# Kernel tuning notes

Measured on AMD Instinct MI355X. Metric: run time of the kernel, lower is better.

Reference implementation:

```python
import jax, jax.numpy as jnp
import numpy as np

B, V, D, H, ET = 32, 50, 6, 256, 4  # batch, num_vars, input_size, decoder_hidden, num_edge_types
E = V * (V - 1)                      # fully connected, no self-loops


def setup_inputs() -> dict:
    key = jax.random.key(0)
    ks = jax.random.split(key, 24)
    s = 0.05
    n = lambda k, shape: jax.random.normal(k, shape, jnp.float32)
    return {
        "inputs": n(ks[0], (B, V, D)),
        "hidden": n(ks[1], (B, V, H)),
        "edges": jax.random.uniform(ks[2], (B, E, ET), jnp.float32),
        # stacked per-edge-type message MLPs for the non-skipped types 1..ET-1
        "W1": n(ks[3], (ET - 1, H, 2 * H)) * s, "b1": jnp.full((ET - 1, H), 0.1, jnp.float32),
        "W2": n(ks[4], (ET - 1, H, H)) * s, "b2": jnp.full((ET - 1, H), 0.1, jnp.float32),
        # GRU-style update (hidden_* have no bias in the torch module)
        "Whr": n(ks[5], (H, H)) * s, "Whi": n(ks[6], (H, H)) * s, "Whh": n(ks[7], (H, H)) * s,
        "Wir": n(ks[8], (H, D)) * s, "bir": jnp.full((H,), 0.1, jnp.float32),
        "Wii": n(ks[9], (H, D)) * s, "bii": jnp.full((H,), 0.1, jnp.float32),
        "Win": n(ks[10], (H, D)) * s, "bin_w": jnp.full((H,), 0.1, jnp.float32),
        # output MLP
        "Wo1": n(ks[11], (H, H)) * s, "bo1": jnp.full((H,), 0.1, jnp.float32),
        "Wo2": n(ks[12], (H, H)) * s, "bo2": jnp.full((H,), 0.1, jnp.float32),
        "Wo3": n(ks[13], (D, H)) * s, "bo3": jnp.full((D,), 0.1, jnp.float32),
    }


def _edge_index(num_vars):
    mask = np.ones((num_vars, num_vars)) - np.eye(num_vars)
    send, recv = np.where(mask)
    onehot = np.zeros((send.shape[0], num_vars), dtype=np.float32)
    onehot[np.arange(send.shape[0]), recv] = 1.0  # edge2node scatter matrix [E, V]
    return send, recv, onehot


def reference(inputs, hidden, edges, W1, b1, W2, b2, Whr, Whi, Whh,
              Wir, bir, Wii, bii, Win, bin_w, Wo1, bo1, Wo2, bo2, Wo3, bo3):
    num_vars = hidden.shape[1]
    send, recv, onehot = _edge_index(num_vars)
    onehot = jnp.asarray(onehot)

    # gather: [B, E, 2H]
    pre_msg = jnp.concatenate([hidden[:, recv, :], hidden[:, send, :]], axis=-1)

    # per-edge-type message MLP (dropout is identity in eval mode), types 1..ET-1 (skip_first)
    m = jnp.tanh(jnp.einsum('bef,thf->bteh', pre_msg, W1) + b1[None, :, None, :])
    m = jnp.tanh(jnp.einsum('bteh,tgh->bteg', m, W2) + b2[None, :, None, :])
    ew = jnp.moveaxis(edges[:, :, 1:], -1, 1)          # [B, T, E]
    norm = edges.shape[-1] - 1
    all_msgs = jnp.einsum('bteh,bte->beh', m, ew) / norm  # [B, E, H]

    # scatter-aggregate edges -> receiver nodes
    agg = jnp.einsum('beh,ev->bvh', all_msgs, onehot) / (num_vars - 1)  # [B, V, H]

    # GRU-style gated update
    r = jax.nn.sigmoid(inputs @ Wir.T + bir + agg @ Whr.T)
    i = jax.nn.sigmoid(inputs @ Wii.T + bii + agg @ Whi.T)
    n_ = jnp.tanh(inputs @ Win.T + bin_w + r * (agg @ Whh.T))
    hidden_new = (1 - i) * n_ + i * hidden

    # output MLP with residual on inputs
    p = jax.nn.relu(hidden_new @ Wo1.T + bo1)
    p = jax.nn.relu(p @ Wo2.T + bo2)
    pred = inputs + (p @ Wo3.T + bo3)
    return pred, hidden_new
```

## Files before the change

### kernel.cpp

```cpp
#include <hip/hip_runtime.h>
#include <hip/hip_bf16.h>
#include <math.h>

#define B_ 32
#define V_ 50
#define D_ 6
#define H_ 256
#define E_ 2450
#define T_ 3
#define NN 1600
#define CHUNKS 39

#define OFF_inputs 0
#define OFF_hidden 9600
#define OFF_edges  419200
#define OFF_W1     732800
#define OFF_b1     1126016
#define OFF_W2     1126784
#define OFF_b2     1323392
#define OFF_Whr    1324160
#define OFF_Whi    1389696
#define OFF_Whh    1455232
#define OFF_Wir    1520768
#define OFF_bir    1522304
#define OFF_Wii    1522560
#define OFF_bii    1524096
#define OFF_Win    1524352
#define OFF_binw   1525888
#define OFF_Wo1    1526144
#define OFF_bo1    1591680
#define OFF_Wo2    1591936
#define OFF_bo2    1657472
#define OFF_Wo3    1657728
#define OFF_bo3    1659264
#define TOTAL_IN   1659270

#define PW_W2   0
#define PW_W1   196608
#define PW_WG   589824
#define PW_WO1  786432
#define PW_WO2  851968
#define PW_HID  917504
#define PW_TOT  1327104
#define AGG_N   409600

typedef __attribute__((ext_vector_type(8))) short short8;
typedef __attribute__((ext_vector_type(4))) float f32x4;

__device__ __forceinline__ float bfc(unsigned int u) {
    return __uint_as_float((u & 0xffffu) << 16);
}
__device__ __forceinline__ unsigned short f2bf(float f) {
    return __builtin_bit_cast(unsigned short, __float2bfloat16(f));
}
__device__ __forceinline__ float tanh_fast(float x) {
    float e = __builtin_amdgcn_exp2f(x * 2.8853900817779268f);
    return 1.0f - 2.0f * __builtin_amdgcn_rcpf(1.0f + e);
}
__device__ __forceinline__ float sigmoid_fast(float x) {
    float e = __builtin_amdgcn_exp2f(x * -1.4426950408889634f);
    return __builtin_amdgcn_rcpf(1.0f + e);
}

struct Ptrs { const void* p[22]; };

__device__ __forceinline__ int detect_bf(const Ptrs& pt) {
    const unsigned short* b1r = (const unsigned short*)pt.p[4];
    return (b1r[0] == 0x3DCDu && b1r[1] == 0x3DCDu) ? 1 : 0;
}
__device__ __forceinline__ float ldraw(const Ptrs& pt, int bf, int ti, int li) {
    return bf ? bfc(((const unsigned short*)pt.p[ti])[li])
              : ((const float*)pt.p[ti])[li];
}

__global__ __launch_bounds__(256) void kprepA(Ptrs pt, float* __restrict__ stag,
                                              unsigned short* __restrict__ W2s,
                                              unsigned short* __restrict__ W1s,
                                              unsigned short* __restrict__ Wgs,
                                              unsigned short* __restrict__ Wo1s,
                                              unsigned short* __restrict__ Wo2s,
                                              unsigned short* __restrict__ hidbf,
                                              float* __restrict__ aggf) {
    int i = blockIdx.x * 256 + threadIdx.x;
    if (i >= TOTAL_IN + PW_TOT + AGG_N) return;
    int bf = detect_bf(pt);
    if (i < TOTAL_IN) {
        int ti, base;
        if      (i < OFF_hidden) { ti = 0;  base = OFF_inputs; }
        else if (i < OFF_edges)  { ti = 1;  base = OFF_hidden; }
        else if (i < OFF_W1)     { ti = 2;  base = OFF_edges;  }
        else if (i < OFF_b1)     { ti = 3;  base = OFF_W1;     }
        else if (i < OFF_W2)     { ti = 4;  base = OFF_b1;     }
        else if (i < OFF_b2)     { ti = 5;  base = OFF_W2;     }
        else if (i < OFF_Whr)    { ti = 6;  base = OFF_b2;     }
        else if (i < OFF_Whi)    { ti = 7;  base = OFF_Whr;    }
        else if (i < OFF_Whh)    { ti = 8;  base = OFF_Whi;    }
        else if (i < OFF_Wir)    { ti = 9;  base = OFF_Whh;    }
        else if (i < OFF_bir)    { ti = 10; base = OFF_Wir;    }
        else if (i < OFF_Wii)    { ti = 11; base = OFF_bir;    }
        else if (i < OFF_bii)    { ti = 12; base = OFF_Wii;    }
        else if (i < OFF_Win)    { ti = 13; base = OFF_bii;    }
        else if (i < OFF_binw)   { ti = 14; base = OFF_Win;    }
        else if (i < OFF_Wo1)    { ti = 15; base = OFF_binw;   }
        else if (i < OFF_bo1)    { ti = 16; base = OFF_Wo1;    }
        else if (i < OFF_Wo2)    { ti = 17; base = OFF_bo1;    }
        else if (i < OFF_bo2)    { ti = 18; base = OFF_Wo2;    }
        else if (i < OFF_Wo3)    { ti = 19; base = OFF_bo2;    }
        else if (i < OFF_bo3)    { ti = 20; base = OFF_Wo3;    }
        else                     { ti = 21; base = OFF_bo3;    }
        stag[i] = ldraw(pt, bf, ti, i - base);
        return;
    }
    int ii = i - TOTAL_IN;
    if (ii < PW_W1) {
        int j = ii & 7, l = (ii >> 3) & 63;
        int rest = ii >> 9;
        int ntg = rest & 15, k0 = (rest >> 4) & 7, t = rest >> 7;
        int g = ntg * 16 + (l & 15);
        int k = k0 * 32 + ((l >> 4) << 3) + j;
        W2s[ii] = f2bf(ldraw(pt, bf, 5, (t * H_ + g) * H_ + k));
    } else if (ii < PW_WG) {
        int i1 = ii - PW_W1;
        int j = i1 & 7, l = (i1 >> 3) & 63;
        int rest = i1 >> 9;
        int ntg = rest % 96, k0 = rest / 96;
        int n = ntg * 16 + (l & 15);
        int t = n >> 9, half = (n >> 8) & 1, h = n & 255;
        int k = k0 * 32 + ((l >> 4) << 3) + j;
        W1s[i1] = f2bf(ldraw(pt, bf, 3, (t * H_ + h) * (2 * H_) + half * H_ + k));
    } else if (ii < PW_WO1) {
        int i2 = ii - PW_WG;
        int j = i2 & 7, l = (i2 >> 3) & 63;
        int rest = i2 >> 9;
        int ntg = rest % 48, k0 = rest / 48;
        int n = ntg * 16 + (l & 15);
        int gate = n >> 8, h = n & 255;
        int k = k0 * 32 + ((l >> 4) << 3) + j;
        Wgs[i2] = f2bf(ldraw(pt, bf, 7 + gate, h * H_ + k));
    } else if (ii < PW_WO2) {
        int i3 = ii - PW_WO1;
        int j = i3 & 7, l = (i3 >> 3) & 63;
        int rest = i3 >> 9;
        int ntg = rest & 15, k0 = rest >> 4;
        int h = ntg * 16 + (l & 15);
        int k = k0 * 32 + ((l >> 4) << 3) + j;
        Wo1s[i3] = f2bf(ldraw(pt, bf, 16, h * H_ + k));
    } else if (ii < PW_HID) {
        int i4 = ii - PW_WO2;
        int j = i4 & 7, l = (i4 >> 3) & 63;
        int rest = i4 >> 9;
        int ntg = rest & 15, k0 = rest >> 4;
        int h = ntg * 16 + (l & 15);
        int k = k0 * 32 + ((l >> 4) << 3) + j;
        Wo2s[i4] = f2bf(ldraw(pt, bf, 18, h * H_ + k));
    } else if (ii < PW_TOT) {
        int i5 = ii - PW_HID;
        hidbf[i5] = f2bf(ldraw(pt, bf, 1, i5));
    } else {
        aggf[ii - PW_TOT] = 0.f;
    }
}

__global__ __launch_bounds__(256) void k1M(const unsigned short* __restrict__ hidbf,
                                           const unsigned short* __restrict__ W1s,
                                           const float* __restrict__ stag,
                                           float* __restrict__ Hr, float* __restrict__ Hs) {
    int m0 = blockIdx.x * 64;
    int nb = blockIdx.y;
    int t = nb >> 1, half = nb & 1;
    int tid = threadIdx.x;
    int w = tid >> 6, l = tid & 63, l15 = l & 15, quad = l >> 4;

    f32x4 acc[4][4];
    #pragma unroll
    for (int mt = 0; mt < 4; mt++)
        #pragma unroll
        for (int nt = 0; nt < 4; nt++) acc[mt][nt] = (f32x4){0.f, 0.f, 0.f, 0.f};

    for (int k0 = 0; k0 < 8; k0++) {
        short8 af[4], bfr[4];
        #pragma unroll
        for (int mt = 0; mt < 4; mt++) {
            int node = m0 + mt * 16 + l15;
            af[mt] = *(const short8*)&hidbf[node * H_ + k0 * 32 + quad * 8];
        }
        #pragma unroll
        for (int nt = 0; nt < 4; nt++) {
            int ntg = nb * 16 + w * 4 + nt;
            bfr[nt] = *(const short8*)&W1s[((k0 * 96 + ntg) << 9) + (l << 3)];
        }
        #pragma unroll
        for (int mt = 0; mt < 4; mt++)
            #pragma unroll
            for (int nt = 0; nt < 4; nt++)
                acc[mt][nt] = __builtin_amdgcn_mfma_f32_16x16x32_bf16(
                    af[mt], bfr[nt], acc[mt][nt], 0, 0, 0);
    }

    float* dst = half ? Hs : Hr;
    #pragma unroll
    for (int mt = 0; mt < 4; mt++)
        #pragma unroll
        for (int nt = 0; nt < 4; nt++) {
            int h = w * 64 + nt * 16 + l15;
            float bias = half ? 0.f : stag[OFF_b1 + t * H_ + h];
            #pragma unroll
            for (int r = 0; r < 4; r++) {
                int node = m0 + mt * 16 + quad * 4 + r;
                dst[((size_t)t * NN + node) * H_ + h] = acc[mt][nt][r] + bias;
            }
        }
}

__global__ __launch_bounds__(512, 6) void k2(const float* __restrict__ stag,
                                             const float* __restrict__ Hr,
                                             const float* __restrict__ Hs,
                                             const unsigned short* __restrict__ W2s,
                                             float* __restrict__ aggf) {
    int c = blockIdx.x, b = blockIdx.y;
    int m0 = c * 64;
    int tid = threadIdx.x;
    int w = tid >> 6, l = tid & 63, l15 = l & 15, quad = l >> 4;
    int mtW = w >> 1, half4 = (w & 1) * 4;

    __shared__ __align__(16) unsigned short m1A[32 * 64 * 8];
    __shared__ float sew[T_][64];

    if (tid < 64) {
        int mR = m0 + tid;
        if (mR < E_) {
            int vv = mR / 49, j = mR - vv * 49;
            int ss = j + (j >= vv ? 1 : 0);
            int e = ss * (V_ - 1) + (vv > ss ? vv - 1 : vv);
            #pragma unroll
            for (int t = 0; t < T_; t++)
                sew[t][tid] = stag[OFF_edges + ((size_t)b * E_ + e) * 4 + 1 + t];
        } else {
            #pragma unroll
            for (int t = 0; t < T_; t++) sew[t][tid] = 0.f;
        }
    }

    int rowT = mtW * 16 + l15;
    int mT_ = m0 + rowT;
    int vThr = 0, sThr = 0;
    if (mT_ < E_) {
        vThr = mT_ / 49; int j = mT_ - vThr * 49;
        sThr = j + (j >= vThr ? 1 : 0);
    }

    int v0 = m0 / 49;
    int B1 = (v0 + 1) * 49, B2 = B1 + 49;

    float tot0 = 0.f, tot1 = 0.f, hi0 = 0.f, hi1 = 0.f, hh0 = 0.f, hh1 = 0.f;

    for (int t = 0; t < T_; t++) {
        const float* hsrow = Hs + (((size_t)t * B_ + b) * V_ + sThr) * H_;
        const float* hrrow = Hr + (((size_t)t * B_ + b) * V_ + vThr) * H_;
        #pragma unroll
        for (int i = 0; i < 4; i++) {
            int k0 = half4 + i;
            int cc = k0 * 32 + quad * 8;
            float4 x0 = *(const float4*)(hsrow + cc);
            float4 h0 = *(const float4*)(hrrow + cc);
            float4 x1 = *(const float4*)(hsrow + cc + 4);
            float4 h1 = *(const float4*)(hrrow + cc + 4);
            unsigned short pk[8];
            pk[0] = f2bf(tanh_fast(x0.x + h0.x));
            pk[1] = f2bf(tanh_fast(x0.y + h0.y));
            pk[2] = f2bf(tanh_fast(x0.z + h0.z));
            pk[3] = f2bf(tanh_fast(x0.w + h0.w));
            pk[4] = f2bf(tanh_fast(x1.x + h1.x));
            pk[5] = f2bf(tanh_fast(x1.y + h1.y));
            pk[6] = f2bf(tanh_fast(x1.z + h1.z));
            pk[7] = f2bf(tanh_fast(x1.w + h1.w));
            *(short8*)&m1A[(((mtW << 3) + k0) << 9) + (l << 3)] = *(short8*)pk;
        }
        __syncthreads();

        f32x4 acc[4][2];
        #pragma unroll
        for (int mt = 0; mt < 4; mt++) {
            acc[mt][0] = (f32x4){0.f, 0.f, 0.f, 0.f};
            acc[mt][1] = (f32x4){0.f, 0.f, 0.f, 0.f};
        }
        __builtin_amdgcn_s_setprio(1);
        for (int k0 = 0; k0 < 8; k0++) {
            int ntg0 = w * 2;
            short8 bf0 = *(const short8*)&W2s[((((t * 8 + k0) * 16 + ntg0) << 6) + l) << 3];
            short8 bf1 = *(const short8*)&W2s[((((t * 8 + k0) * 16 + ntg0 + 1) << 6) + l) << 3];
            #pragma unroll
            for (int mt = 0; mt < 4; mt++) {
                short8 af = *(const short8*)&m1A[(((mt << 3) + k0) << 9) + (l << 3)];
                acc[mt][0] = __builtin_amdgcn_mfma_f32_16x16x32_bf16(af, bf0, acc[mt][0], 0, 0, 0);
                acc[mt][1] = __builtin_amdgcn_mfma_f32_16x16x32_bf16(af, bf1, acc[mt][1], 0, 0, 0);
            }
        }
        __builtin_amdgcn_s_setprio(0);

        float b2v0 = stag[OFF_b2 + t * H_ + (w * 2) * 16 + l15];
        float b2v1 = stag[OFF_b2 + t * H_ + (w * 2 + 1) * 16 + l15];
        #pragma unroll
        for (int mt = 0; mt < 4; mt++) {
            #pragma unroll
            for (int r = 0; r < 4; r++) {
                int row = mt * 16 + quad * 4 + r;
                int m = m0 + row;
                float ewv = sew[t][row];
                float c0 = ewv * tanh_fast(acc[mt][0][r] + b2v0);
                float c1 = ewv * tanh_fast(acc[mt][1][r] + b2v1);
                tot0 += c0; tot1 += c1;
                hi0 += (m >= B1) ? c0 : 0.f;
                hi1 += (m >= B1) ? c1 : 0.f;
                hh0 += (m >= B2) ? c0 : 0.f;
                hh1 += (m >= B2) ? c1 : 0.f;
            }
        }
        __syncthreads();
    }

    float s00 = tot0 - hi0, s01 = tot1 - hi1;
    float s10 = hi0 - hh0,  s11 = hi1 - hh1;
    s00 += __shfl_xor(s00, 16, 64); s00 += __shfl_xor(s00, 32, 64);
    s01 += __shfl_xor(s01, 16, 64); s01 += __shfl_xor(s01, 32, 64);
    s10 += __shfl_xor(s10, 16, 64); s10 += __shfl_xor(s10, 32, 64);
    s11 += __shfl_xor(s11, 16, 64); s11 += __shfl_xor(s11, 32, 64);
    hh0 += __shfl_xor(hh0, 16, 64); hh0 += __shfl_xor(hh0, 32, 64);
    hh1 += __shfl_xor(hh1, 16, 64); hh1 += __shfl_xor(hh1, 32, 64);

    if (quad == 0) {
        const float scale = 1.0f / ((float)T_ * (float)(V_ - 1));
        int col0 = (w * 2) * 16 + l15;
        size_t base0 = ((size_t)b * V_ + v0) * H_;
        atomicAdd(&aggf[base0 + col0], s00 * scale);
        atomicAdd(&aggf[base0 + col0 + 16], s01 * scale);
        if (B1 < m0 + 64) {
            int v1c = min(v0 + 1, V_ - 1);
            size_t base1 = ((size_t)b * V_ + v1c) * H_;
            atomicAdd(&aggf[base1 + col0], s10 * scale);
            atomicAdd(&aggf[base1 + col0 + 16], s11 * scale);
        }
        if (B2 < m0 + 64) {
            int v2c = min(v0 + 2, V_ - 1);
            size_t base2 = ((size_t)b * V_ + v2c) * H_;
            atomicAdd(&aggf[base2 + col0], hh0 * scale);
            atomicAdd(&aggf[base2 + col0 + 16], hh1 * scale);
        }
    }
}

__global__ __launch_bounds__(256) void k4f(Ptrs pt, const float* __restrict__ stag,
                                           const float* __restrict__ aggf,
                                           const unsigned short* __restrict__ Wgs,
                                           const unsigned short* __restrict__ Wo1s,
                                           const unsigned short* __restrict__ Wo2s,
                                           void* __restrict__ dout) {
    int n0 = blockIdx.x * 16;
    int tid = threadIdx.x;
    int w = tid >> 6, l = tid & 63, l15 = l & 15, quad = l >> 4;
    int bf = detect_bf(pt);

    __shared__ __align__(16) unsigned short bufA[16][264];
    __shared__ __align__(16) unsigned short bufB[16][264];

    f32x4 acc[3][4];
    #pragma unroll
    for (int g = 0; g < 3; g++)
        #pragma unroll
        for (int nt = 0; nt < 4; nt++) acc[g][nt] = (f32x4){0.f, 0.f, 0.f, 0.f};

    for (int k0 = 0; k0 < 8; k0++) {
        const float* ar = aggf + (size_t)(n0 + l15) * H_ + k0 * 32 + quad * 8;
        float4 q0 = *(const float4*)ar;
        float4 q1 = *(const float4*)(ar + 4);
        unsigned short pk[8];
        pk[0] = f2bf(q0.x); pk[1] = f2bf(q0.y); pk[2] = f2bf(q0.z); pk[3] = f2bf(q0.w);
        pk[4] = f2bf(q1.x); pk[5] = f2bf(q1.y); pk[6] = f2bf(q1.z); pk[7] = f2bf(q1.w);
        short8 af = *(const short8*)pk;
        #pragma unroll
        for (int g = 0; g < 3; g++)
            #pragma unroll
            for (int nt = 0; nt < 4; nt++) {
                int ntg = g * 16 + w * 4 + nt;
                short8 bfr = *(const short8*)&Wgs[((k0 * 48 + ntg) << 9) + (l << 3)];
                acc[g][nt] = __builtin_amdgcn_mfma_f32_16x16x32_bf16(
                    af, bfr, acc[g][nt], 0, 0, 0);
            }
    }

    float inp[4][D_];
    #pragma unroll
    for (int r = 0; r < 4; r++) {
        int node = n0 + quad * 4 + r;
        #pragma unroll
        for (int d = 0; d < D_; d++) inp[r][d] = stag[OFF_inputs + node * D_ + d];
    }
    #pragma unroll
    for (int nt = 0; nt < 4; nt++) {
        int h = w * 64 + nt * 16 + l15;
        float wir[D_], wii[D_], win[D_];
        #pragma unroll
        for (int d = 0; d < D_; d++) {
            wir[d] = stag[OFF_Wir + h * D_ + d];
            wii[d] = stag[OFF_Wii + h * D_ + d];
            win[d] = stag[OFF_Win + h * D_ + d];
        }
        float br = stag[OFF_bir + h], bi = stag[OFF_bii + h], bn = stag[OFF_binw + h];
        #pragma unroll
        for (int r = 0; r < 4; r++) {
            int node = n0 + quad * 4 + r;
            float xr = br, xi = bi, xn = bn;
            #pragma unroll
            for (int d = 0; d < D_; d++) {
                xr += inp[r][d] * wir[d];
                xi += inp[r][d] * wii[d];
                xn += inp[r][d] * win[d];
            }
            float rg = sigmoid_fast(xr + acc[0][nt][r]);
            float ig = sigmoid_fast(xi + acc[1][nt][r]);
            float ng = tanh_fast(xn + rg * acc[2][nt][r]);
            float hprev = stag[OFF_hidden + (size_t)node * H_ + h];
            float hn = (1.f - ig) * ng + ig * hprev;
            unsigned short hb = f2bf(hn);
            bufA[quad * 4 + r][h] = hb;
            if (bf) ((unsigned short*)dout)[9600 + (size_t)node * H_ + h] = hb;
            else    ((float*)dout)[9600 + (size_t)node * H_ + h] = hn;
        }
    }
    __syncthreads();

    {
        f32x4 a1[4];
        #pragma unroll
        for (int nt = 0; nt < 4; nt++) a1[nt] = (f32x4){0.f, 0.f, 0.f, 0.f};
        for (int k0 = 0; k0 < 8; k0++) {
            short8 af = *(const short8*)&bufA[l15][k0 * 32 + quad * 8];
            #pragma unroll
            for (int nt = 0; nt < 4; nt++) {
                int ntg = w * 4 + nt;
                short8 bfr = *(const short8*)&Wo1s[((k0 * 16 + ntg) << 9) + (l << 3)];
                a1[nt] = __builtin_amdgcn_mfma_f32_16x16x32_bf16(af, bfr, a1[nt], 0, 0, 0);
            }
        }
        __syncthreads();
        #pragma unroll
        for (int nt = 0; nt < 4; nt++) {
            int h = w * 64 + nt * 16 + l15;
            float bo = stag[OFF_bo1 + h];
            #pragma unroll
            for (int r = 0; r < 4; r++)
                bufB[quad * 4 + r][h] = f2bf(fmaxf(a1[nt][r] + bo, 0.f));
        }
    }
    __syncthreads();

    {
        f32x4 a2[4];
        #pragma unroll
        for (int nt = 0; nt < 4; nt++) a2[nt] = (f32x4){0.f, 0.f, 0.f, 0.f};
        for (int k0 = 0; k0 < 8; k0++) {
            short8 af = *(const short8*)&bufB[l15][k0 * 32 + quad * 8];
            #pragma unroll
            for (int nt = 0; nt < 4; nt++) {
                int ntg = w * 4 + nt;
                short8 bfr = *(const short8*)&Wo2s[((k0 * 16 + ntg) << 9) + (l << 3)];
                a2[nt] = __builtin_amdgcn_mfma_f32_16x16x32_bf16(af, bfr, a2[nt], 0, 0, 0);
            }
        }
        __syncthreads();
        #pragma unroll
        for (int nt = 0; nt < 4; nt++) {
            int h = w * 64 + nt * 16 + l15;
            float bo = stag[OFF_bo2 + h];
            #pragma unroll
            for (int r = 0; r < 4; r++)
                bufA[quad * 4 + r][h] = f2bf(fmaxf(a2[nt][r] + bo, 0.f));
        }
    }
    __syncthreads();

    if (tid < 16 * D_) {
        int nl = tid / D_, d = tid % D_;
        const float* wrow = stag + OFF_Wo3 + d * H_;
        float a = stag[OFF_bo3 + d];
        for (int k = 0; k < H_; k += 8) {
            short8 pv = *(const short8*)&bufA[nl][k];
            float4 w0 = *(const float4*)(wrow + k);
            float4 w1 = *(const float4*)(wrow + k + 4);
            a += bfc((unsigned short)pv[0]) * w0.x + bfc((unsigned short)pv[1]) * w0.y
               + bfc((unsigned short)pv[2]) * w0.z + bfc((unsigned short)pv[3]) * w0.w
               + bfc((unsigned short)pv[4]) * w1.x + bfc((unsigned short)pv[5]) * w1.y
               + bfc((unsigned short)pv[6]) * w1.z + bfc((unsigned short)pv[7]) * w1.w;
        }
        int node = n0 + nl;
        float val = a + stag[OFF_inputs + node * D_ + d];
        if (bf) ((unsigned short*)dout)[node * D_ + d] = f2bf(val);
        else    ((float*)dout)[node * D_ + d] = val;
    }
}

extern "C" void kernel_launch(void* const* d_in, const int* in_sizes, int n_in,
                              void* d_out, int out_size, void* d_ws, size_t ws_size,
                              hipStream_t stream) {
    float* stag = (float*)d_ws;
    float* Hr   = stag + 1659272;
    float* Hs   = Hr + 1228800;
    float* aggf = Hs + 1228800;
    unsigned short* W2s   = (unsigned short*)(aggf + 409600);
    unsigned short* W1s   = (unsigned short*)((float*)W2s + 98304);
    unsigned short* Wgs   = (unsigned short*)((float*)W1s + 196608);
    unsigned short* Wo1s  = (unsigned short*)((float*)Wgs + 98304);
    unsigned short* Wo2s  = (unsigned short*)((float*)Wo1s + 32768);
    unsigned short* hidbf = (unsigned short*)((float*)Wo2s + 32768);

    Ptrs pt;
    for (int i = 0; i < 22; i++) pt.p[i] = d_in[i];

    kprepA<<<(TOTAL_IN + PW_TOT + AGG_N + 255) / 256, 256, 0, stream>>>(
        pt, stag, W2s, W1s, Wgs, Wo1s, Wo2s, hidbf, aggf);
    k1M<<<dim3(25, 6), 256, 0, stream>>>(hidbf, W1s, stag, Hr, Hs);
    k2<<<dim3(CHUNKS, B_), 512, 0, stream>>>(stag, Hr, Hs, W2s, aggf);
    k4f<<<NN / 16, 256, 0, stream>>>(pt, stag, aggf, Wgs, Wo1s, Wo2s, d_out);
}
```

Measured before the change: 228.1 us.

## Replace atomic aggregation with per-chunk partial sums and remap k2 block order

The edge kernel no longer atomically adds into a zeroed node-aggregate buffer. Each chunk block now writes up to three per-node partial rows to a scratch buffer, and the update kernel sums the one or two partials that cover each node. This drops the zero-fill pass from the prep kernel and the atomic contention. The k2 block index is also remapped so consecutive blocks are spread across the XCDs. In exchange the workspace grows and the update kernel does extra conditional loads.

```diff
diff --git a/kernel.cpp b/kernel.cpp
--- a/kernel.cpp
+++ b/kernel.cpp
@@ -42,7 +42,6 @@
 #define PW_WO2  851968
 #define PW_HID  917504
 #define PW_TOT  1327104
-#define AGG_N   409600
 
 typedef __attribute__((ext_vector_type(8))) short short8;
 typedef __attribute__((ext_vector_type(4))) float f32x4;
@@ -79,10 +78,9 @@
                                               unsigned short* __restrict__ Wgs,
                                               unsigned short* __restrict__ Wo1s,
                                               unsigned short* __restrict__ Wo2s,
-                                              unsigned short* __restrict__ hidbf,
-                                              float* __restrict__ aggf) {
+                                              unsigned short* __restrict__ hidbf) {
     int i = blockIdx.x * 256 + threadIdx.x;
-    if (i >= TOTAL_IN + PW_TOT + AGG_N) return;
+    if (i >= TOTAL_IN + PW_TOT) return;
     int bf = detect_bf(pt);
     if (i < TOTAL_IN) {
         int ti, base;
@@ -153,11 +151,9 @@
         int h = ntg * 16 + (l & 15);
         int k = k0 * 32 + ((l >> 4) << 3) + j;
         Wo2s[i4] = f2bf(ldraw(pt, bf, 18, h * H_ + k));
-    } else if (ii < PW_TOT) {
+    } else {
         int i5 = ii - PW_HID;
         hidbf[i5] = f2bf(ldraw(pt, bf, 1, i5));
-    } else {
-        aggf[ii - PW_TOT] = 0.f;
     }
 }
 
@@ -216,8 +212,10 @@
                                              const float* __restrict__ Hr,
                                              const float* __restrict__ Hs,
                                              const unsigned short* __restrict__ W2s,
-                                             float* __restrict__ aggf) {
-    int c = blockIdx.x, b = blockIdx.y;
+                                             float* __restrict__ aggp) {
+    int flat = blockIdx.y * CHUNKS + blockIdx.x;
+    int wg = (flat & 7) * 156 + (flat >> 3);
+    int b = wg / CHUNKS, c = wg - b * CHUNKS;
     int m0 = c * 64;
     int tid = threadIdx.x;
     int w = tid >> 6, l = tid & 63, l15 = l & 15, quad = l >> 4;
@@ -331,26 +329,18 @@
     if (quad == 0) {
         const float scale = 1.0f / ((float)T_ * (float)(V_ - 1));
         int col0 = (w * 2) * 16 + l15;
-        size_t base0 = ((size_t)b * V_ + v0) * H_;
-        atomicAdd(&aggf[base0 + col0], s00 * scale);
-        atomicAdd(&aggf[base0 + col0 + 16], s01 * scale);
-        if (B1 < m0 + 64) {
-            int v1c = min(v0 + 1, V_ - 1);
-            size_t base1 = ((size_t)b * V_ + v1c) * H_;
-            atomicAdd(&aggf[base1 + col0], s10 * scale);
-            atomicAdd(&aggf[base1 + col0 + 16], s11 * scale);
-        }
-        if (B2 < m0 + 64) {
-            int v2c = min(v0 + 2, V_ - 1);
-            size_t base2 = ((size_t)b * V_ + v2c) * H_;
-            atomicAdd(&aggf[base2 + col0], hh0 * scale);
-            atomicAdd(&aggf[base2 + col0 + 16], hh1 * scale);
-        }
+        float* pb = aggp + ((size_t)(b * CHUNKS + c) * 3) * H_;
+        pb[col0]            = s00 * scale;
+        pb[col0 + 16]       = s01 * scale;
+        pb[H_ + col0]       = s10 * scale;
+        pb[H_ + col0 + 16]  = s11 * scale;
+        pb[2*H_ + col0]      = hh0 * scale;
+        pb[2*H_ + col0 + 16] = hh1 * scale;
     }
 }
 
 __global__ __launch_bounds__(256) void k4f(Ptrs pt, const float* __restrict__ stag,
-                                           const float* __restrict__ aggf,
+                                           const float* __restrict__ aggp,
                                            const unsigned short* __restrict__ Wgs,
                                            const unsigned short* __restrict__ Wo1s,
                                            const unsigned short* __restrict__ Wo2s,
@@ -363,6 +353,16 @@
     __shared__ __align__(16) unsigned short bufA[16][264];
     __shared__ __align__(16) unsigned short bufB[16][264];
 
+    int nodeA = n0 + l15;
+    int bA = nodeA / V_, vA = nodeA - bA * V_;
+    int clo = (49 * vA) >> 6;
+    int chi = (49 * vA + 48) >> 6;
+    int seglo = vA - (clo * 64) / 49;
+    int seghi = vA - (chi * 64) / 49;
+    const float* p1 = aggp + ((size_t)(bA * CHUNKS + clo) * 3 + seglo) * H_;
+    const float* p2 = aggp + ((size_t)(bA * CHUNKS + chi) * 3 + seghi) * H_;
+    bool two = (chi != clo);
+
     f32x4 acc[3][4];
     #pragma unroll
     for (int g = 0; g < 3; g++)
@@ -370,9 +370,15 @@
         for (int nt = 0; nt < 4; nt++) acc[g][nt] = (f32x4){0.f, 0.f, 0.f, 0.f};
 
     for (int k0 = 0; k0 < 8; k0++) {
-        const float* ar = aggf + (size_t)(n0 + l15) * H_ + k0 * 32 + quad * 8;
-        float4 q0 = *(const float4*)ar;
-        float4 q1 = *(const float4*)(ar + 4);
+        int koff = k0 * 32 + quad * 8;
+        float4 q0 = *(const float4*)(p1 + koff);
+        float4 q1 = *(const float4*)(p1 + koff + 4);
+        if (two) {
+            float4 r0 = *(const float4*)(p2 + koff);
+            float4 r1 = *(const float4*)(p2 + koff + 4);
+            q0.x += r0.x; q0.y += r0.y; q0.z += r0.z; q0.w += r0.w;
+            q1.x += r1.x; q1.y += r1.y; q1.z += r1.z; q1.w += r1.w;
+        }
         unsigned short pk[8];
         pk[0] = f2bf(q0.x); pk[1] = f2bf(q0.y); pk[2] = f2bf(q0.z); pk[3] = f2bf(q0.w);
         pk[4] = f2bf(q1.x); pk[5] = f2bf(q1.y); pk[6] = f2bf(q1.z); pk[7] = f2bf(q1.w);
@@ -505,8 +511,8 @@
     float* stag = (float*)d_ws;
     float* Hr   = stag + 1659272;
     float* Hs   = Hr + 1228800;
-    float* aggf = Hs + 1228800;
-    unsigned short* W2s   = (unsigned short*)(aggf + 409600);
+    float* aggp = Hs + 1228800;
+    unsigned short* W2s   = (unsigned short*)(aggp + 958464);
     unsigned short* W1s   = (unsigned short*)((float*)W2s + 98304);
     unsigned short* Wgs   = (unsigned short*)((float*)W1s + 196608);
     unsigned short* Wo1s  = (unsigned short*)((float*)Wgs + 98304);
@@ -516,9 +522,9 @@
     Ptrs pt;
     for (int i = 0; i < 22; i++) pt.p[i] = d_in[i];
 
-    kprepA<<<(TOTAL_IN + PW_TOT + AGG_N + 255) / 256, 256, 0, stream>>>(
-        pt, stag, W2s, W1s, Wgs, Wo1s, Wo2s, hidbf, aggf);
+    kprepA<<<(TOTAL_IN + PW_TOT + 255) / 256, 256, 0, stream>>>(
+        pt, stag, W2s, W1s, Wgs, Wo1s, Wo2s, hidbf);
     k1M<<<dim3(25, 6), 256, 0, stream>>>(hidbf, W1s, stag, Hr, Hs);
-    k2<<<dim3(CHUNKS, B_), 512, 0, stream>>>(stag, Hr, Hs, W2s, aggf);
-    k4f<<<NN / 16, 256, 0, stream>>>(pt, stag, aggf, Wgs, Wo1s, Wo2s, d_out);
-}
+    k2<<<dim3(CHUNKS, B_), 512, 0, stream>>>(stag, Hr, Hs, W2s, aggp);
+    k4f<<<NN / 16, 256, 0, stream>>>(pt, stag, aggp, Wgs, Wo1s, Wo2s, d_out);
+}
```

New measurement: 236.1 us. 3.5% more time.
